# Kernel tuning notes

Measured on AMD Instinct MI355X. Metric: run time of the kernel, lower is better.

The kernel has to match this reference:

```python
import jax, jax.numpy as jnp
import numpy as np

T = 25
H1, H2, H3 = 16, 72, 32


def _lin_params(key, out_dim, in_dim):
    k1, k2 = jax.random.split(key)
    s = 1.0 / np.sqrt(in_dim)
    W = jax.random.uniform(k1, (out_dim, in_dim), jnp.float32, -s, s)
    b = jax.random.uniform(k2, (out_dim,), jnp.float32, -s, s)
    return W, b


def _lstm_params(key, in_dim, hid):
    k1, k2, k3, k4 = jax.random.split(key, 4)
    s = 1.0 / np.sqrt(hid)
    Wih = jax.random.uniform(k1, (4 * hid, in_dim), jnp.float32, -s, s)
    Whh = jax.random.uniform(k2, (4 * hid, hid), jnp.float32, -s, s)
    bih = jax.random.uniform(k3, (4 * hid,), jnp.float32, -s, s)
    bhh = jax.random.uniform(k4, (4 * hid,), jnp.float32, -s, s)
    return Wih, Whh, bih, bhh


def setup_inputs() -> dict:
    key = jax.random.key(0)
    ks = jax.random.split(key, 9)
    B = 131072
    x = jax.random.normal(ks[0], (B, T, 2), jnp.float32)
    y = jax.random.normal(ks[1], (B, T, 36), jnp.float32)
    Wih1, Whh1, bih1, bhh1 = _lstm_params(ks[2], 2, H1)
    Wih2, Whh2, bih2, bhh2 = _lstm_params(ks[3], H2, H2)
    Wih3, Whh3, bih3, bhh3 = _lstm_params(ks[4], H1 + H2, H3)
    W1, b1 = _lin_params(ks[5], 64, 36)
    W2, b2 = _lin_params(ks[6], H2, 64)
    W3, b3 = _lin_params(ks[7], 16, H3)
    W4, b4 = _lin_params(ks[8], 2, 16)
    return dict(x=x, y=y,
                Wih1=Wih1, Whh1=Whh1, bih1=bih1, bhh1=bhh1,
                Wih2=Wih2, Whh2=Whh2, bih2=bih2, bhh2=bhh2,
                Wih3=Wih3, Whh3=Whh3, bih3=bih3, bhh3=bhh3,
                W1=W1, b1=b1, W2=W2, b2=b2, W3=W3, b3=b3, W4=W4, b4=b4)


def _lstm_cell(xt, h, c, Wih, Whh, bih, bhh):
    # PyTorch LSTMCell gate order: i, f, g, o
    g = xt @ Wih.T + bih + h @ Whh.T + bhh
    i, f, gg, o = jnp.split(g, 4, axis=-1)
    c_new = jax.nn.sigmoid(f) * c + jax.nn.sigmoid(i) * jnp.tanh(gg)
    h_new = jax.nn.sigmoid(o) * jnp.tanh(c_new)
    return h_new, c_new


def _forward(x, y, Wih1, Whh1, bih1, bhh1, Wih2, Whh2, bih2, bhh2,
             Wih3, Whh3, bih3, bhh3, W1, b1, W2, b2, W3, b3, W4, b4):
    B = x.shape[0]
    init = (jnp.zeros((B, H1), jnp.float32), jnp.zeros((B, H1), jnp.float32),
            jnp.zeros((B, H2), jnp.float32), jnp.zeros((B, H2), jnp.float32),
            jnp.zeros((B, H3), jnp.float32), jnp.zeros((B, H3), jnp.float32))

    def step(carry, inp):
        h1, c1, h2, c2, h3, c3 = carry
        xt, yt = inp  # [B,2], [B,36]
        h1, c1 = _lstm_cell(xt, h1, c1, Wih1, Whh1, bih1, bhh1)
        l2 = jax.nn.relu(yt @ W1.T + b1) @ W2.T + b2
        h2, c2 = _lstm_cell(l2, h2, c2, Wih2, Whh2, bih2, bhh2)
        h = jnp.concatenate([h1, h2], axis=1)
        h3, c3 = _lstm_cell(h, h3, c3, Wih3, Whh3, bih3, bhh3)
        out = jax.nn.relu(h3 @ W3.T + b3) @ W4.T + b4  # [B,2]
        return (h1, c1, h2, c2, h3, c3), out

    xs = (jnp.swapaxes(x, 0, 1), jnp.swapaxes(y, 0, 1))  # [T,B,*]
    _, outs = jax.lax.scan(step, init, xs)  # [T,B,2]
    # torch.cat(outputs, dim=1) -> [B, T*2]
    return jnp.swapaxes(outs, 0, 1).reshape(B, T * 2)


def reference(x, y, Wih1, Whh1, bih1, bhh1, Wih2, Whh2, bih2, bhh2,
              Wih3, Whh3, bih3, bhh3, W1, b1, W2, b2, W3, b3, W4, b4):
    return _forward(x, y, Wih1, Whh1, bih1, bhh1, Wih2, Whh2, bih2, bhh2,
                    Wih3, Whh3, bih3, bhh3, W1, b1, W2, b2, W3, b3, W4, b4)
```

## Files before the change

### kernel.cpp

```cpp
#include <hip/hip_runtime.h>
#include <hip/hip_bf16.h>

#define THREADS 768

typedef __hip_bfloat16 bf16;
typedef __attribute__((ext_vector_type(4))) float f32x4;
typedef __attribute__((ext_vector_type(8))) short bf16x8;

#define MFMA __builtin_amdgcn_mfma_f32_16x16x32_bf16

#define O_A1  0
#define O_AY  4096
#define O_AT1 12288
#define O_A2  20480
#define O_AH3 40960
#define LDS_ELEMS 45056
#define LDS_BYTES (LDS_ELEMS * 2)

__device__ __forceinline__ int kmap(int l, int j) {
    return (((l >> 4) & 3) << 2) + (j & 3) + ((j >> 2) << 4);
}
__device__ __forceinline__ int frag_off(int m, int k) {
    int l = (m & 15) | (((k >> 2) & 3) << 4);
    int j = (k & 3) | (((k >> 4) & 1) << 2);
    return (l << 3) + j;
}
__device__ __forceinline__ void st_frag(bf16* sbase, int KC, int m, int k, float v) {
    sbase[(((m >> 4) * KC + (k >> 5)) << 9) + frag_off(m, k & 31)] = __float2bfloat16(v);
}
__device__ __forceinline__ void st_frag_c(bf16* sbase, int KC, int m, int cidx, int kl, float v) {
    sbase[(((m >> 4) * KC + cidx) << 9) + frag_off(m, kl)] = __float2bfloat16(v);
}

__device__ __forceinline__ float rcp_(float x) { return __builtin_amdgcn_rcpf(x); }

__device__ __forceinline__ float lstm_ew1(f32x4 acc, float& cst) {
    float ei = __expf(-acc[0]);
    float ef = __expf(-acc[1]);
    float eg = __expf(2.0f * fminf(acc[2], 40.0f));
    float eo = __expf(-acc[3]);
    float c = rcp_(1.0f + ef) * cst + (eg - 1.0f) * rcp_((1.0f + ei) * (eg + 1.0f));
    cst = c;
    float ec = __expf(2.0f * fminf(c, 40.0f));
    return (ec - 1.0f) * rcp_((1.0f + eo) * (ec + 1.0f));
}

__device__ __forceinline__ ushort bfu(float f) {
    union { bf16 b; ushort u; } v; v.b = __float2bfloat16(f); return v.u;
}

template <typename F>
__device__ __forceinline__ bf16x8 mk_frag(int lane, F val) {
    union { bf16x8 v; bf16 h[8]; } u;
#pragma unroll
    for (int j = 0; j < 8; ++j) u.h[j] = __float2bfloat16(val(kmap(lane, j)));
    return u.v;
}

__global__ void __launch_bounds__(THREADS, 3)
lstm_fused(const float* __restrict__ x, const float* __restrict__ y,
           const float* __restrict__ Wih1, const float* __restrict__ Whh1,
           const float* __restrict__ bih1, const float* __restrict__ bhh1,
           const float* __restrict__ Wih2, const float* __restrict__ Whh2,
           const float* __restrict__ bih2, const float* __restrict__ bhh2,
           const float* __restrict__ Wih3, const float* __restrict__ Whh3,
           const float* __restrict__ bih3, const float* __restrict__ bhh3,
           const float* __restrict__ W1, const float* __restrict__ b1,
           const float* __restrict__ W2, const float* __restrict__ b2,
           const float* __restrict__ W3, const float* __restrict__ b3,
           const float* __restrict__ W4, const float* __restrict__ b4,
           float* __restrict__ out) {
    extern __shared__ char smem[];
    bf16* sb = (bf16*)smem;
    const int tid = threadIdx.x;
    const int wave = tid >> 6, lane = tid & 63, ln15 = lane & 15;
    const int b0 = blockIdx.x * 64;

    const bool HEAVY = wave < 6;
    const int ntL2a = HEAVY ? 2 * wave : 6 + wave;

    bf16x8 bL2[2][5];
    bf16x8 bL1 = {};
    bf16x8 bF1[2] = {};
    bf16x8 bF2[2] = {};
    bf16x8 bL3[5] = {};
    bf16x8 bF3 = {};

    {
        auto fillL2 = [&](int nt, bf16x8* dst) {
            int R = (nt << 4) + ln15;
            int r = (R & 3) * 72 + (R >> 2);
            float bias = bih2[r] + bhh2[r];
#pragma unroll
            for (int kc = 0; kc < 5; ++kc)
                dst[kc] = mk_frag(lane, [&](int kl) {
                    int k = kc * 32 + kl;
                    return k < 72 ? Wih2[r * 72 + k]
                         : (k < 144 ? Whh2[r * 72 + (k - 72)]
                         : (k == 144 ? bias : 0.0f)); });
        };
        fillL2(ntL2a, bL2[0]);
        if (HEAVY) fillL2(2 * wave + 1, bL2[1]);
        else { bL2[1][0] = bL2[0][0]; bL2[1][1] = bL2[0][0]; bL2[1][2] = bL2[0][0];
               bL2[1][3] = bL2[0][0]; bL2[1][4] = bL2[0][0]; }
    }
    if (wave >= 6 && wave < 10) {
        int R = ((wave - 6) << 4) + ln15;
        int r = (R & 3) * 16 + (R >> 2);
        float bias = bih1[r] + bhh1[r];
        bL1 = mk_frag(lane, [&](int k) {
            return k < 2 ? Wih1[r * 2 + k]
                 : (k < 18 ? Whh1[r * 16 + (k - 2)]
                 : (k == 18 ? bias : 0.0f)); });
    }
    if (wave >= 8) {
        int n = ((wave - 8) << 4) + ln15;
        float bias = b1[n];
#pragma unroll
        for (int kc = 0; kc < 2; ++kc)
            bF1[kc] = mk_frag(lane, [&](int kl) {
                int k = kc * 32 + kl;
                return k < 36 ? W1[n * 36 + k] : (k == 36 ? bias : 0.0f); });
    }
    if (wave >= 4) {
        int R = ((wave - 4) << 4) + ln15;
        int r = (R & 3) * 32 + (R >> 2);
        float bias = bih3[r] + bhh3[r];
        bL3[0] = mk_frag(lane, [&](int k) {
            return (k >= 2 && k < 18) ? Wih3[r * 88 + (k - 2)] : (k == 18 ? bias : 0.0f); });
        bL3[1] = mk_frag(lane, [&](int k) {
            return (k >= 8) ? Wih3[r * 88 + 8 + k] : 0.0f; });
        bL3[2] = mk_frag(lane, [&](int k) { return Wih3[r * 88 + 40 + k]; });
        bL3[3] = mk_frag(lane, [&](int k) {
            return (k < 16) ? Wih3[r * 88 + 72 + k] : 0.0f; });
        bL3[4] = mk_frag(lane, [&](int k) { return Whh3[r * 32 + k]; });
    }
    if (wave < 4 || wave == 7) {
        int nt2 = (wave == 7) ? 4 : wave;
        int n = (nt2 << 4) + ln15;
#pragma unroll
        for (int kc = 0; kc < 2; ++kc)
            bF2[kc] = mk_frag(lane, [&](int kl) {
                return (n < 72) ? W2[n * 64 + kc * 32 + kl] : 0.0f; });
    }
    if (wave < 4) bF3 = mk_frag(lane, [&](int k) { return W3[ln15 * 32 + k]; });

    {
        int4* z = (int4*)sb;
        int4 zv = {0, 0, 0, 0};
        for (int i = tid; i < LDS_BYTES / 16; i += THREADS) z[i] = zv;
    }
    __syncthreads();
    for (int it = tid; it < 2 * 2304; it += THREADS) {
        int slot = it / 2304, r2 = it - slot * 2304;
        int m = r2 / 36, k = r2 - m * 36;
        st_frag(sb + O_AY + ((slot * 8) << 9), 2, m, k,
                y[(size_t)(b0 + m) * 900 + slot * 36 + k]);
    }
    if (tid < 128) {
        int m = tid >> 1, k = tid & 1;
        st_frag(sb + O_A1, 1, m, k, x[(size_t)(b0 + m) * 50 + k]);
    }
    {
        const bf16 one = __float2bfloat16(1.0f);
        if (tid < 128) {
            int s = tid >> 6, mt = (tid >> 4) & 3, n = tid & 15;
            sb[O_A1 + ((s * 4 + mt) << 9) + frag_off(n, 18)] = one;
        } else if (tid < 256) {
            int i = tid - 128; int s = i >> 6, mt = (i >> 4) & 3, n = i & 15;
            sb[O_AY + ((s * 8 + mt * 2 + 1) << 9) + frag_off(n, 4)] = one;
        } else if (tid < 384) {
            int i = tid - 256; int s = i >> 6, mt = (i >> 4) & 3, n = i & 15;
            sb[O_A2 + ((mt * 10 + 8 + s) << 9) + frag_off(n, 16)] = one;
        }
    }
    __syncthreads();
    if (wave >= 8) {
        const int nf0 = ((wave - 8) << 4) + ((lane >> 4) << 2);
#pragma unroll
        for (int s = 0; s < 2; ++s) {
#pragma unroll
            for (int mt = 0; mt < 4; ++mt) {
                f32x4 acc = {0.f, 0.f, 0.f, 0.f};
#pragma unroll
                for (int kc = 0; kc < 2; ++kc) {
                    bf16x8 a = *(const bf16x8*)(sb + O_AY + ((s * 8 + mt * 2 + kc) << 9) + (lane << 3));
                    acc = MFMA(bF1[kc], a, acc, 0, 0, 0);
                }
                int batch = (mt << 4) + ln15;
#pragma unroll
                for (int r = 0; r < 4; ++r)
                    st_frag(sb + O_AT1 + (((s ^ 1) * 8) << 9), 2, batch, nf0 + r, fmaxf(acc[r], 0.0f));
            }
        }
    }
    __syncthreads();
    if (wave < 4 || wave == 7) {
        const int nt2 = (wave == 7) ? 4 : wave;
        const int nb = (nt2 << 4) + ((lane >> 4) << 2);
        float4 bv = {0.f, 0.f, 0.f, 0.f};
        if (nb < 72) bv = *(const float4*)(b2 + nb);
#pragma unroll
        for (int mt = 0; mt < 4; ++mt) {
            f32x4 acc = {0.f, 0.f, 0.f, 0.f};
#pragma unroll
            for (int kc = 0; kc < 2; ++kc) {
                bf16x8 a = *(const bf16x8*)(sb + O_AT1 + ((8 + mt * 2 + kc) << 9) + (lane << 3));
                acc = MFMA(bF2[kc], a, acc, 0, 0, 0);
            }
            if (nb < 72) {
                int batch = (mt << 4) + ln15;
#pragma unroll
                for (int r = 0; r < 4; ++r) {
                    int n = nb + r;
                    st_frag_c(sb + O_A2, 10, batch, ((n >> 5) << 1), n & 31, acc[r] + bv[r]);
                }
            }
        }
    } else if (wave >= 10) {
        const int m = ((wave - 10) << 5) + (lane >> 1);
        const int mt = m >> 4;
        const float* yp = y + (size_t)(b0 + m) * 900 + 2 * 36;
#pragma unroll
        for (int c = (lane & 1); c < 9; c += 2) {
            float4 v = *(const float4*)(yp + 4 * c);
            ushort4 pk;
            pk.x = bfu(v.x); pk.y = bfu(v.y); pk.z = bfu(v.z); pk.w = bfu(v.w);
            int k0 = 4 * c, kc = k0 >> 5;
            int l2v = (m & 15) | (((k0 >> 2) & 3) << 4);
            int j0 = ((k0 >> 4) & 1) << 2;
            *(ushort4*)((ushort*)(sb + O_AY) + ((mt * 2 + kc) << 9) + (l2v << 3) + j0) = pk;
        }
    }
    float c1[4] = {};
    float cs2[2][4] = {};
    float c3[4] = {};
    __syncthreads();

    for (int t = 0; t <= 25; ++t) {
        const int p = t & 1, q = p ^ 1;

        if (t <= 24) {
#pragma unroll
            for (int mt = 0; mt < 4; ++mt) {
                bf16x8 al[5];
#pragma unroll
                for (int b = 0; b < 5; ++b)
                    al[b] = *(const bf16x8*)(sb + O_A2 + ((mt * 10 + 2 * b + p) << 9) + (lane << 3));
                {
                    f32x4 acc = {0.f, 0.f, 0.f, 0.f};
#pragma unroll
                    for (int b = 0; b < 5; ++b) acc = MFMA(bL2[0][b], al[b], acc, 0, 0, 0);
                    float hv = lstm_ew1(acc, cs2[0][mt]);
                    int batch = (mt << 4) + ln15;
                    int k = 72 + (ntL2a << 2) + (lane >> 4);
                    st_frag_c(sb + O_A2, 10, batch, ((k >> 5) << 1) + q, k & 31, hv);
                }
                if (HEAVY) {
                    f32x4 acc = {0.f, 0.f, 0.f, 0.f};
#pragma unroll
                    for (int b = 0; b < 5; ++b) acc = MFMA(bL2[1][b], al[b], acc, 0, 0, 0);
                    float hv = lstm_ew1(acc, cs2[1][mt]);
                    int batch = (mt << 4) + ln15;
                    int k = 72 + ((2 * wave + 1) << 2) + (lane >> 4);
                    st_frag_c(sb + O_A2, 10, batch, ((k >> 5) << 1) + q, k & 31, hv);
                }
            }
        }

        if (t <= 24 && wave >= 6 && wave < 10) {
            const int nt1 = wave - 6;
#pragma unroll
            for (int mt = 0; mt < 4; ++mt) {
                bf16x8 a = *(const bf16x8*)(sb + O_A1 + ((p * 4 + mt) << 9) + (lane << 3));
                f32x4 acc = {0.f, 0.f, 0.f, 0.f};
                acc = MFMA(bL1, a, acc, 0, 0, 0);
                float hv = lstm_ew1(acc, c1[mt]);
                int batch = (mt << 4) + ln15;
                st_frag(sb + O_A1 + ((q * 4) << 9), 1, batch, 2 + (nt1 << 2) + (lane >> 4), hv);
            }
        }
        if (wave == 6 && t <= 23) {
            const int m = lane, mt = m >> 4;
            float2 xv = *(const float2*)(x + (size_t)(b0 + m) * 50 + (t + 1) * 2);
            union { uint u; ushort s[2]; } xu;
            xu.s[0] = bfu(xv.x); xu.s[1] = bfu(xv.y);
            *(uint*)((ushort*)(sb + O_A1) + ((q * 4 + mt) << 9) + ((m & 15) << 3)) = xu.u;
        }
        if (t <= 22 && wave >= 8) {
            const int nf0 = ((wave - 8) << 4) + ((lane >> 4) << 2);
#pragma unroll
            for (int mt = 0; mt < 4; ++mt) {
                f32x4 acc = {0.f, 0.f, 0.f, 0.f};
#pragma unroll
                for (int kc = 0; kc < 2; ++kc) {
                    bf16x8 a = *(const bf16x8*)(sb + O_AY + ((p * 8 + mt * 2 + kc) << 9) + (lane << 3));
                    acc = MFMA(bF1[kc], a, acc, 0, 0, 0);
                }
                int batch = (mt << 4) + ln15;
#pragma unroll
                for (int r = 0; r < 4; ++r)
                    st_frag(sb + O_AT1 + ((q * 8) << 9), 2, batch, nf0 + r, fmaxf(acc[r], 0.0f));
            }
        }
        if (wave >= 10 && t <= 21) {
            const int m = ((wave - 10) << 5) + (lane >> 1);
            const int mt = m >> 4;
            const float* yp = y + (size_t)(b0 + m) * 900 + (t + 3) * 36;
#pragma unroll
            for (int c = (lane & 1); c < 9; c += 2) {
                float4 v = *(const float4*)(yp + 4 * c);
                ushort4 pk;
                pk.x = bfu(v.x); pk.y = bfu(v.y); pk.z = bfu(v.z); pk.w = bfu(v.w);
                int k0 = 4 * c, kc = k0 >> 5;
                int l2v = (m & 15) | (((k0 >> 2) & 3) << 4);
                int j0 = ((k0 >> 4) & 1) << 2;
                *(ushort4*)((ushort*)(sb + O_AY) + ((q * 8 + mt * 2 + kc) << 9) + (l2v << 3) + j0) = pk;
            }
        }
        if (t >= 1 && wave >= 4) {
            const int nt3 = wave - 4;
#pragma unroll
            for (int mt = 0; mt < 4; ++mt) {
                f32x4 acc = {0.f, 0.f, 0.f, 0.f};
                bf16x8 a0 = *(const bf16x8*)(sb + O_A1 + ((p * 4 + mt) << 9) + (lane << 3));
                acc = MFMA(bL3[0], a0, acc, 0, 0, 0);
#pragma unroll
                for (int j = 0; j < 3; ++j) {
                    bf16x8 a = *(const bf16x8*)(sb + O_A2 + ((mt * 10 + 4 + 2 * j + p) << 9) + (lane << 3));
                    acc = MFMA(bL3[1 + j], a, acc, 0, 0, 0);
                }
                bf16x8 a4 = *(const bf16x8*)(sb + O_AH3 + ((p * 4 + mt) << 9) + (lane << 3));
                acc = MFMA(bL3[4], a4, acc, 0, 0, 0);
                float hv = lstm_ew1(acc, c3[mt]);
                int batch = (mt << 4) + ln15;
                st_frag(sb + O_AH3 + ((q * 4) << 9), 1, batch, (nt3 << 2) + (lane >> 4), hv);
            }
        }
        if (t <= 23 && (wave < 4 || wave == 7)) {
            const int nt2 = (wave == 7) ? 4 : wave;
            const int nb = (nt2 << 4) + ((lane >> 4) << 2);
            float4 bv = {0.f, 0.f, 0.f, 0.f};
            if (nb < 72) bv = *(const float4*)(b2 + nb);
#pragma unroll
            for (int mt = 0; mt < 4; ++mt) {
                f32x4 acc = {0.f, 0.f, 0.f, 0.f};
#pragma unroll
                for (int kc = 0; kc < 2; ++kc) {
                    bf16x8 a = *(const bf16x8*)(sb + O_AT1 + ((p * 8 + mt * 2 + kc) << 9) + (lane << 3));
                    acc = MFMA(bF2[kc], a, acc, 0, 0, 0);
                }
                if (nb < 72) {
                    int batch = (mt << 4) + ln15;
#pragma unroll
                    for (int r = 0; r < 4; ++r) {
                        int n = nb + r;
                        st_frag_c(sb + O_A2, 10, batch, ((n >> 5) << 1) + q, n & 31, acc[r] + bv[r]);
                    }
                }
            }
        }
        if (t >= 2 && wave < 4) {
            const int mt = wave, qd = lane >> 4;
            float4 b3v = *(const float4*)(b3 + 4 * qd);
            float4 w0v = *(const float4*)(W4 + 4 * qd);
            float4 w1v = *(const float4*)(W4 + 16 + 4 * qd);
            bf16x8 bb = *(const bf16x8*)(sb + O_AH3 + ((p * 4 + mt) << 9) + (lane << 3));
            f32x4 acc = {0.f, 0.f, 0.f, 0.f};
            acc = MFMA(bF3, bb, acc, 0, 0, 0);
            float s0 = 0.f, s1 = 0.f;
#pragma unroll
            for (int r = 0; r < 4; ++r) {
                float u = fmaxf(acc[r] + b3v[r], 0.0f);
                s0 = fmaf(u, w0v[r], s0);
                s1 = fmaf(u, w1v[r], s1);
            }
            s0 += __shfl_xor(s0, 16); s0 += __shfl_xor(s0, 32);
            s1 += __shfl_xor(s1, 16); s1 += __shfl_xor(s1, 32);
            if (lane < 16) {
                float2 o; o.x = s0 + b4[0]; o.y = s1 + b4[1];
                *(float2*)(out + (size_t)(b0 + (mt << 4) + lane) * 50 + (t - 2) * 2) = o;
            }
        }
        __syncthreads();
    }

    if (wave < 4) {
        const int mt = wave, qd = lane >> 4;
        float4 b3v = *(const float4*)(b3 + 4 * qd);
        float4 w0v = *(const float4*)(W4 + 4 * qd);
        float4 w1v = *(const float4*)(W4 + 16 + 4 * qd);
        bf16x8 bb = *(const bf16x8*)(sb + O_AH3 + (mt << 9) + (lane << 3));
        f32x4 acc = {0.f, 0.f, 0.f, 0.f};
        acc = MFMA(bF3, bb, acc, 0, 0, 0);
        float s0 = 0.f, s1 = 0.f;
#pragma unroll
        for (int r = 0; r < 4; ++r) {
            float u = fmaxf(acc[r] + b3v[r], 0.0f);
            s0 = fmaf(u, w0v[r], s0);
            s1 = fmaf(u, w1v[r], s1);
        }
        s0 += __shfl_xor(s0, 16); s0 += __shfl_xor(s0, 32);
        s1 += __shfl_xor(s1, 16); s1 += __shfl_xor(s1, 32);
        if (lane < 16) {
            float2 o; o.x = s0 + b4[0]; o.y = s1 + b4[1];
            *(float2*)(out + (size_t)(b0 + (mt << 4) + lane) * 50 + 24 * 2) = o;
        }
    }
}

extern "C" void kernel_launch(void* const* d_in, const int* in_sizes, int n_in,
                              void* d_out, int out_size, void* d_ws, size_t ws_size,
                              hipStream_t stream) {
    (void)in_sizes; (void)n_in; (void)d_ws; (void)ws_size; (void)out_size;
    hipFuncSetAttribute((const void*)lstm_fused,
                        hipFuncAttributeMaxDynamicSharedMemorySize, LDS_BYTES);
    lstm_fused<<<dim3(2048), dim3(THREADS), LDS_BYTES, stream>>>(
        (const float*)d_in[0], (const float*)d_in[1],
        (const float*)d_in[2], (const float*)d_in[3],
        (const float*)d_in[4], (const float*)d_in[5],
        (const float*)d_in[6], (const float*)d_in[7],
        (const float*)d_in[8], (const float*)d_in[9],
        (const float*)d_in[10], (const float*)d_in[11],
        (const float*)d_in[12], (const float*)d_in[13],
        (const float*)d_in[14], (const float*)d_in[15],
        (const float*)d_in[16], (const float*)d_in[17],
        (const float*)d_in[18], (const float*)d_in[19],
        (const float*)d_in[20], (const float*)d_in[21],
        (float*)d_out);
}
```

Before: 1.001 ms.

## Rebalance LSTM work across 16 waves with unified per-wave weight register array

The block grows from 12 to 16 waves, and all layers' work is reassigned across them. L2 gate tiles now go to waves 0-13, L1 to waves 4-7 and L3 to waves 8-15, while the dense y→l2 path runs on waves 14-15 plus wave 4. Per-wave weight fragments are collapsed into a single 13-entry register array so that each wave holds only the fragments for its roles, keeping register pressure within the tighter 1024-thread launch bound. The goal is a shorter per-timestep critical path through better load balance, at the cost of more waves per block contending for the barriers and the MFMA units.

New measurement: 1.013 ms. No clear change (+1.1%).

```diff
diff --git a/kernel.cpp b/kernel.cpp
--- a/kernel.cpp
+++ b/kernel.cpp
@@ -1,7 +1,7 @@
 #include <hip/hip_runtime.h>
 #include <hip/hip_bf16.h>
 
-#define THREADS 768
+#define THREADS 1024
 
 typedef __hip_bfloat16 bf16;
 typedef __attribute__((ext_vector_type(4))) float f32x4;
@@ -57,7 +57,7 @@
     return u.v;
 }
 
-__global__ void __launch_bounds__(THREADS, 3)
+__global__ void __launch_bounds__(THREADS, 4)
 lstm_fused(const float* __restrict__ x, const float* __restrict__ y,
            const float* __restrict__ Wih1, const float* __restrict__ Whh1,
            const float* __restrict__ bih1, const float* __restrict__ bhh1,
@@ -76,74 +76,82 @@
     const int wave = tid >> 6, lane = tid & 63, ln15 = lane & 15;
     const int b0 = blockIdx.x * 64;
 
-    const bool HEAVY = wave < 6;
-    const int ntL2a = HEAVY ? 2 * wave : 6 + wave;
-
-    bf16x8 bL2[2][5];
-    bf16x8 bL1 = {};
-    bf16x8 bF1[2] = {};
-    bf16x8 bF2[2] = {};
-    bf16x8 bL3[5] = {};
-    bf16x8 bF3 = {};
+    bf16x8 W[13];
+#pragma unroll
+    for (int i = 0; i < 13; ++i) W[i] = bf16x8{0, 0, 0, 0, 0, 0, 0, 0};
 
     {
-        auto fillL2 = [&](int nt, bf16x8* dst) {
+        auto l2frag = [&](int nt, int kc) {
             int R = (nt << 4) + ln15;
             int r = (R & 3) * 72 + (R >> 2);
             float bias = bih2[r] + bhh2[r];
-#pragma unroll
-            for (int kc = 0; kc < 5; ++kc)
-                dst[kc] = mk_frag(lane, [&](int kl) {
-                    int k = kc * 32 + kl;
-                    return k < 72 ? Wih2[r * 72 + k]
-                         : (k < 144 ? Whh2[r * 72 + (k - 72)]
-                         : (k == 144 ? bias : 0.0f)); });
+            return mk_frag(lane, [&](int kl) {
+                int k = kc * 32 + kl;
+                return k < 72 ? Wih2[r * 72 + k]
+                     : (k < 144 ? Whh2[r * 72 + (k - 72)]
+                     : (k == 144 ? bias : 0.0f)); });
         };
-        fillL2(ntL2a, bL2[0]);
-        if (HEAVY) fillL2(2 * wave + 1, bL2[1]);
-        else { bL2[1][0] = bL2[0][0]; bL2[1][1] = bL2[0][0]; bL2[1][2] = bL2[0][0];
-               bL2[1][3] = bL2[0][0]; bL2[1][4] = bL2[0][0]; }
-    }
-    if (wave >= 6 && wave < 10) {
-        int R = ((wave - 6) << 4) + ln15;
+        if (wave < 4) {
+#pragma unroll
+            for (int kc = 0; kc < 5; ++kc) W[kc] = l2frag(2 * wave, kc);
+#pragma unroll
+            for (int kc = 0; kc < 5; ++kc) W[5 + kc] = l2frag(2 * wave + 1, kc);
+        } else if (wave < 14) {
+#pragma unroll
+            for (int kc = 0; kc < 5; ++kc) W[kc] = l2frag(wave + 4, kc);
+        }
+    }
+    if (wave >= 4 && wave < 8) {
+        int R = ((wave - 4) << 4) + ln15;
         int r = (R & 3) * 16 + (R >> 2);
         float bias = bih1[r] + bhh1[r];
-        bL1 = mk_frag(lane, [&](int k) {
+        W[5] = mk_frag(lane, [&](int k) {
             return k < 2 ? Wih1[r * 2 + k]
                  : (k < 18 ? Whh1[r * 16 + (k - 2)]
                  : (k == 18 ? bias : 0.0f)); });
     }
-    if (wave >= 8) {
-        int n = ((wave - 8) << 4) + ln15;
-        float bias = b1[n];
+    if (wave == 4) {
+        int n = 64 + ln15;
 #pragma unroll
         for (int kc = 0; kc < 2; ++kc)
-            bF1[kc] = mk_frag(lane, [&](int kl) {
-                int k = kc * 32 + kl;
-                return k < 36 ? W1[n * 36 + k] : (k == 36 ? bias : 0.0f); });
-    }
-    if (wave >= 4) {
-        int R = ((wave - 4) << 4) + ln15;
-        int r = (R & 3) * 32 + (R >> 2);
-        float bias = bih3[r] + bhh3[r];
-        bL3[0] = mk_frag(lane, [&](int k) {
-            return (k >= 2 && k < 18) ? Wih3[r * 88 + (k - 2)] : (k == 18 ? bias : 0.0f); });
-        bL3[1] = mk_frag(lane, [&](int k) {
-            return (k >= 8) ? Wih3[r * 88 + 8 + k] : 0.0f; });
-        bL3[2] = mk_frag(lane, [&](int k) { return Wih3[r * 88 + 40 + k]; });
-        bL3[3] = mk_frag(lane, [&](int k) {
-            return (k < 16) ? Wih3[r * 88 + 72 + k] : 0.0f; });
-        bL3[4] = mk_frag(lane, [&](int k) { return Whh3[r * 32 + k]; });
-    }
-    if (wave < 4 || wave == 7) {
-        int nt2 = (wave == 7) ? 4 : wave;
-        int n = (nt2 << 4) + ln15;
-#pragma unroll
-        for (int kc = 0; kc < 2; ++kc)
-            bF2[kc] = mk_frag(lane, [&](int kl) {
+            W[6 + kc] = mk_frag(lane, [&](int kl) {
                 return (n < 72) ? W2[n * 64 + kc * 32 + kl] : 0.0f; });
     }
-    if (wave < 4) bF3 = mk_frag(lane, [&](int k) { return W3[ln15 * 32 + k]; });
+    {
+        auto l3fill = [&](int base) {
+            int R = ((wave - 8) << 4) + ln15;
+            int r = (R & 3) * 32 + (R >> 2);
+            float bias = bih3[r] + bhh3[r];
+            W[base + 0] = mk_frag(lane, [&](int k) {
+                return (k >= 2 && k < 18) ? Wih3[r * 88 + (k - 2)] : (k == 18 ? bias : 0.0f); });
+            W[base + 1] = mk_frag(lane, [&](int k) {
+                return (k >= 8) ? Wih3[r * 88 + 8 + k] : 0.0f; });
+            W[base + 2] = mk_frag(lane, [&](int k) { return Wih3[r * 88 + 40 + k]; });
+            W[base + 3] = mk_frag(lane, [&](int k) {
+                return (k < 16) ? Wih3[r * 88 + 72 + k] : 0.0f; });
+            W[base + 4] = mk_frag(lane, [&](int k) { return Whh3[r * 32 + k]; });
+        };
+        if (wave >= 8 && wave < 14) l3fill(5);
+        else if (wave >= 14) l3fill(0);
+    }
+    if (wave >= 8 && wave < 12)
+        W[10] = mk_frag(lane, [&](int k) { return W3[ln15 * 32 + k]; });
+    if (wave >= 14) {
+#pragma unroll
+        for (int nn = 0; nn < 2; ++nn) {
+            int n = ((2 * (wave - 14) + nn) << 4) + ln15;
+            float bias = b1[n];
+#pragma unroll
+            for (int kc = 0; kc < 2; ++kc)
+                W[5 + 2 * nn + kc] = mk_frag(lane, [&](int kl) {
+                    int k = kc * 32 + kl;
+                    return k < 36 ? W1[n * 36 + k] : (k == 36 ? bias : 0.0f); });
+#pragma unroll
+            for (int kc = 0; kc < 2; ++kc)
+                W[9 + 2 * nn + kc] = mk_frag(lane, [&](int kl) {
+                    return W2[n * 64 + kc * 32 + kl]; });
+        }
+    }
 
     {
         int4* z = (int4*)sb;
@@ -175,40 +183,40 @@
         }
     }
     __syncthreads();
-    if (wave >= 8) {
-        const int nf0 = ((wave - 8) << 4) + ((lane >> 4) << 2);
-#pragma unroll
-        for (int s = 0; s < 2; ++s) {
+    if (wave >= 14) {
+#pragma unroll
+        for (int nn = 0; nn < 2; ++nn) {
+            const int nf0 = ((2 * (wave - 14) + nn) << 4) + ((lane >> 4) << 2);
+#pragma unroll
+            for (int s = 0; s < 2; ++s) {
+#pragma unroll
+                for (int mt = 0; mt < 4; ++mt) {
+                    f32x4 acc = {0.f, 0.f, 0.f, 0.f};
+                    bf16x8 a0 = *(const bf16x8*)(sb + O_AY + ((s * 8 + mt * 2 + 0) << 9) + (lane << 3));
+                    bf16x8 a1 = *(const bf16x8*)(sb + O_AY + ((s * 8 + mt * 2 + 1) << 9) + (lane << 3));
+                    acc = MFMA(W[5 + 2 * nn], a0, acc, 0, 0, 0);
+                    acc = MFMA(W[6 + 2 * nn], a1, acc, 0, 0, 0);
+                    int batch = (mt << 4) + ln15;
+#pragma unroll
+                    for (int r = 0; r < 4; ++r)
+                        st_frag(sb + O_AT1 + (((s ^ 1) * 8) << 9), 2, batch, nf0 + r, fmaxf(acc[r], 0.0f));
+                }
+            }
+        }
+    }
+    __syncthreads();
+    if (wave >= 14) {
+#pragma unroll
+        for (int nn = 0; nn < 2; ++nn) {
+            const int nb = ((2 * (wave - 14) + nn) << 4) + ((lane >> 4) << 2);
+            float4 bv = *(const float4*)(b2 + nb);
 #pragma unroll
             for (int mt = 0; mt < 4; ++mt) {
                 f32x4 acc = {0.f, 0.f, 0.f, 0.f};
-#pragma unroll
-                for (int kc = 0; kc < 2; ++kc) {
-                    bf16x8 a = *(const bf16x8*)(sb + O_AY + ((s * 8 + mt * 2 + kc) << 9) + (lane << 3));
-                    acc = MFMA(bF1[kc], a, acc, 0, 0, 0);
-                }
-                int batch = (mt << 4) + ln15;
-#pragma unroll
-                for (int r = 0; r < 4; ++r)
-                    st_frag(sb + O_AT1 + (((s ^ 1) * 8) << 9), 2, batch, nf0 + r, fmaxf(acc[r], 0.0f));
-            }
-        }
-    }
-    __syncthreads();
-    if (wave < 4 || wave == 7) {
-        const int nt2 = (wave == 7) ? 4 : wave;
-        const int nb = (nt2 << 4) + ((lane >> 4) << 2);
-        float4 bv = {0.f, 0.f, 0.f, 0.f};
-        if (nb < 72) bv = *(const float4*)(b2 + nb);
-#pragma unroll
-        for (int mt = 0; mt < 4; ++mt) {
-            f32x4 acc = {0.f, 0.f, 0.f, 0.f};
-#pragma unroll
-            for (int kc = 0; kc < 2; ++kc) {
-                bf16x8 a = *(const bf16x8*)(sb + O_AT1 + ((8 + mt * 2 + kc) << 9) + (lane << 3));
-                acc = MFMA(bF2[kc], a, acc, 0, 0, 0);
-            }
-            if (nb < 72) {
+                bf16x8 a0 = *(const bf16x8*)(sb + O_AT1 + ((8 + mt * 2 + 0) << 9) + (lane << 3));
+                bf16x8 a1 = *(const bf16x8*)(sb + O_AT1 + ((8 + mt * 2 + 1) << 9) + (lane << 3));
+                acc = MFMA(W[9 + 2 * nn], a0, acc, 0, 0, 0);
+                acc = MFMA(W[10 + 2 * nn], a1, acc, 0, 0, 0);
                 int batch = (mt << 4) + ln15;
 #pragma unroll
                 for (int r = 0; r < 4; ++r) {
@@ -217,8 +225,7 @@
                 }
             }
         }
-    } else if (wave >= 10) {
-        const int m = ((wave - 10) << 5) + (lane >> 1);
+        const int m = ((wave - 14) << 5) + (lane >> 1);
         const int mt = m >> 4;
         const float* yp = y + (size_t)(b0 + m) * 900 + 2 * 36;
 #pragma unroll
@@ -231,16 +238,58 @@
             int j0 = ((k0 >> 4) & 1) << 2;
             *(ushort4*)((ushort*)(sb + O_AY) + ((mt * 2 + kc) << 9) + (l2v << 3) + j0) = pk;
         }
-    }
-    float c1[4] = {};
-    float cs2[2][4] = {};
-    float c3[4] = {};
+    } else if (wave == 4) {
+        const int nb = 64 + ((lane >> 4) << 2);
+        float4 bv = {0.f, 0.f, 0.f, 0.f};
+        if (nb < 72) bv = *(const float4*)(b2 + nb);
+#pragma unroll
+        for (int mt = 0; mt < 4; ++mt) {
+            f32x4 acc = {0.f, 0.f, 0.f, 0.f};
+            bf16x8 a0 = *(const bf16x8*)(sb + O_AT1 + ((8 + mt * 2 + 0) << 9) + (lane << 3));
+            bf16x8 a1 = *(const bf16x8*)(sb + O_AT1 + ((8 + mt * 2 + 1) << 9) + (lane << 3));
+            acc = MFMA(W[6], a0, acc, 0, 0, 0);
+            acc = MFMA(W[7], a1, acc, 0, 0, 0);
+            if (nb < 72) {
+                int batch = (mt << 4) + ln15;
+#pragma unroll
+                for (int r = 0; r < 4; ++r) {
+                    int n = nb + r;
+                    st_frag_c(sb + O_A2, 10, batch, ((n >> 5) << 1), n & 31, acc[r] + bv[r]);
+                }
+            }
+        }
+    }
+    float cA[4] = {};
+    float cB[4] = {};
     __syncthreads();
+
+#define L3_BODY(W0, W1, W2_, W3_, W4_, CST)                                              \
+    {                                                                                     \
+        const int nt3 = wave - 8;                                                         \
+        _Pragma("unroll")                                                                 \
+        for (int mt = 0; mt < 4; ++mt) {                                                  \
+            f32x4 acc = {0.f, 0.f, 0.f, 0.f};                                             \
+            bf16x8 a0 = *(const bf16x8*)(sb + O_A1 + ((p * 4 + mt) << 9) + (lane << 3));  \
+            acc = MFMA(W0, a0, acc, 0, 0, 0);                                             \
+            bf16x8 a1 = *(const bf16x8*)(sb + O_A2 + ((mt * 10 + 4 + p) << 9) + (lane << 3)); \
+            acc = MFMA(W1, a1, acc, 0, 0, 0);                                             \
+            bf16x8 a2 = *(const bf16x8*)(sb + O_A2 + ((mt * 10 + 6 + p) << 9) + (lane << 3)); \
+            acc = MFMA(W2_, a2, acc, 0, 0, 0);                                            \
+            bf16x8 a3 = *(const bf16x8*)(sb + O_A2 + ((mt * 10 + 8 + p) << 9) + (lane << 3)); \
+            acc = MFMA(W3_, a3, acc, 0, 0, 0);                                            \
+            bf16x8 a4 = *(const bf16x8*)(sb + O_AH3 + ((p * 4 + mt) << 9) + (lane << 3)); \
+            acc = MFMA(W4_, a4, acc, 0, 0, 0);                                            \
+            float hv = lstm_ew1(acc, CST[mt]);                                            \
+            int batch = (mt << 4) + ln15;                                                 \
+            st_frag(sb + O_AH3 + ((q * 4) << 9), 1, batch, (nt3 << 2) + (lane >> 4), hv); \
+        }                                                                                 \
+    }
 
     for (int t = 0; t <= 25; ++t) {
         const int p = t & 1, q = p ^ 1;
 
-        if (t <= 24) {
+        if (t <= 24 && wave < 14) {
+            const int ntA = (wave < 4) ? 2 * wave : wave + 4;
 #pragma unroll
             for (int mt = 0; mt < 4; ++mt) {
                 bf16x8 al[5];
@@ -250,17 +299,17 @@
                 {
                     f32x4 acc = {0.f, 0.f, 0.f, 0.f};
 #pragma unroll
-                    for (int b = 0; b < 5; ++b) acc = MFMA(bL2[0][b], al[b], acc, 0, 0, 0);
-                    float hv = lstm_ew1(acc, cs2[0][mt]);
+                    for (int b = 0; b < 5; ++b) acc = MFMA(W[b], al[b], acc, 0, 0, 0);
+                    float hv = lstm_ew1(acc, cA[mt]);
                     int batch = (mt << 4) + ln15;
-                    int k = 72 + (ntL2a << 2) + (lane >> 4);
+                    int k = 72 + (ntA << 2) + (lane >> 4);
                     st_frag_c(sb + O_A2, 10, batch, ((k >> 5) << 1) + q, k & 31, hv);
                 }
-                if (HEAVY) {
+                if (wave < 4) {
                     f32x4 acc = {0.f, 0.f, 0.f, 0.f};
 #pragma unroll
-                    for (int b = 0; b < 5; ++b) acc = MFMA(bL2[1][b], al[b], acc, 0, 0, 0);
-                    float hv = lstm_ew1(acc, cs2[1][mt]);
+                    for (int b = 0; b < 5; ++b) acc = MFMA(W[5 + b], al[b], acc, 0, 0, 0);
+                    float hv = lstm_ew1(acc, cB[mt]);
                     int batch = (mt << 4) + ln15;
                     int k = 72 + ((2 * wave + 1) << 2) + (lane >> 4);
                     st_frag_c(sb + O_A2, 10, batch, ((k >> 5) << 1) + q, k & 31, hv);
@@ -268,43 +317,45 @@
             }
         }
 
-        if (t <= 24 && wave >= 6 && wave < 10) {
-            const int nt1 = wave - 6;
+        if (t <= 24 && wave >= 4 && wave < 8) {
+            const int nt1 = wave - 4;
 #pragma unroll
             for (int mt = 0; mt < 4; ++mt) {
                 bf16x8 a = *(const bf16x8*)(sb + O_A1 + ((p * 4 + mt) << 9) + (lane << 3));
                 f32x4 acc = {0.f, 0.f, 0.f, 0.f};
-                acc = MFMA(bL1, a, acc, 0, 0, 0);
-                float hv = lstm_ew1(acc, c1[mt]);
+                acc = MFMA(W[5], a, acc, 0, 0, 0);
+                float hv = lstm_ew1(acc, cB[mt]);
                 int batch = (mt << 4) + ln15;
                 st_frag(sb + O_A1 + ((q * 4) << 9), 1, batch, 2 + (nt1 << 2) + (lane >> 4), hv);
             }
         }
-        if (wave == 6 && t <= 23) {
+        if (wave == 5 && t <= 23) {
             const int m = lane, mt = m >> 4;
             float2 xv = *(const float2*)(x + (size_t)(b0 + m) * 50 + (t + 1) * 2);
             union { uint u; ushort s[2]; } xu;
             xu.s[0] = bfu(xv.x); xu.s[1] = bfu(xv.y);
             *(uint*)((ushort*)(sb + O_A1) + ((q * 4 + mt) << 9) + ((m & 15) << 3)) = xu.u;
         }
-        if (t <= 22 && wave >= 8) {
-            const int nf0 = ((wave - 8) << 4) + ((lane >> 4) << 2);
-#pragma unroll
-            for (int mt = 0; mt < 4; ++mt) {
-                f32x4 acc = {0.f, 0.f, 0.f, 0.f};
-#pragma unroll
-                for (int kc = 0; kc < 2; ++kc) {
-                    bf16x8 a = *(const bf16x8*)(sb + O_AY + ((p * 8 + mt * 2 + kc) << 9) + (lane << 3));
-                    acc = MFMA(bF1[kc], a, acc, 0, 0, 0);
-                }
-                int batch = (mt << 4) + ln15;
-#pragma unroll
-                for (int r = 0; r < 4; ++r)
-                    st_frag(sb + O_AT1 + ((q * 8) << 9), 2, batch, nf0 + r, fmaxf(acc[r], 0.0f));
-            }
-        }
-        if (wave >= 10 && t <= 21) {
-            const int m = ((wave - 10) << 5) + (lane >> 1);
+        if (t <= 22 && wave >= 14) {
+#pragma unroll
+            for (int nn = 0; nn < 2; ++nn) {
+                const int nf0 = ((2 * (wave - 14) + nn) << 4) + ((lane >> 4) << 2);
+#pragma unroll
+                for (int mt = 0; mt < 4; ++mt) {
+                    f32x4 acc = {0.f, 0.f, 0.f, 0.f};
+                    bf16x8 a0 = *(const bf16x8*)(sb + O_AY + ((p * 8 + mt * 2 + 0) << 9) + (lane << 3));
+                    bf16x8 a1 = *(const bf16x8*)(sb + O_AY + ((p * 8 + mt * 2 + 1) << 9) + (lane << 3));
+                    acc = MFMA(W[5 + 2 * nn], a0, acc, 0, 0, 0);
+                    acc = MFMA(W[6 + 2 * nn], a1, acc, 0, 0, 0);
+                    int batch = (mt << 4) + ln15;
+#pragma unroll
+                    for (int r = 0; r < 4; ++r)
+                        st_frag(sb + O_AT1 + ((q * 8) << 9), 2, batch, nf0 + r, fmaxf(acc[r], 0.0f));
+                }
+            }
+        }
+        if (wave >= 14 && t <= 21) {
+            const int m = ((wave - 14) << 5) + (lane >> 1);
             const int mt = m >> 4;
             const float* yp = y + (size_t)(b0 + m) * 900 + (t + 3) * 36;
 #pragma unroll
@@ -318,56 +369,61 @@
                 *(ushort4*)((ushort*)(sb + O_AY) + ((q * 8 + mt * 2 + kc) << 9) + (l2v << 3) + j0) = pk;
             }
         }
-        if (t >= 1 && wave >= 4) {
-            const int nt3 = wave - 4;
-#pragma unroll
-            for (int mt = 0; mt < 4; ++mt) {
-                f32x4 acc = {0.f, 0.f, 0.f, 0.f};
-                bf16x8 a0 = *(const bf16x8*)(sb + O_A1 + ((p * 4 + mt) << 9) + (lane << 3));
-                acc = MFMA(bL3[0], a0, acc, 0, 0, 0);
-#pragma unroll
-                for (int j = 0; j < 3; ++j) {
-                    bf16x8 a = *(const bf16x8*)(sb + O_A2 + ((mt * 10 + 4 + 2 * j + p) << 9) + (lane << 3));
-                    acc = MFMA(bL3[1 + j], a, acc, 0, 0, 0);
-                }
-                bf16x8 a4 = *(const bf16x8*)(sb + O_AH3 + ((p * 4 + mt) << 9) + (lane << 3));
-                acc = MFMA(bL3[4], a4, acc, 0, 0, 0);
-                float hv = lstm_ew1(acc, c3[mt]);
-                int batch = (mt << 4) + ln15;
-                st_frag(sb + O_AH3 + ((q * 4) << 9), 1, batch, (nt3 << 2) + (lane >> 4), hv);
-            }
-        }
-        if (t <= 23 && (wave < 4 || wave == 7)) {
-            const int nt2 = (wave == 7) ? 4 : wave;
-            const int nb = (nt2 << 4) + ((lane >> 4) << 2);
-            float4 bv = {0.f, 0.f, 0.f, 0.f};
-            if (nb < 72) bv = *(const float4*)(b2 + nb);
-#pragma unroll
-            for (int mt = 0; mt < 4; ++mt) {
-                f32x4 acc = {0.f, 0.f, 0.f, 0.f};
-#pragma unroll
-                for (int kc = 0; kc < 2; ++kc) {
-                    bf16x8 a = *(const bf16x8*)(sb + O_AT1 + ((p * 8 + mt * 2 + kc) << 9) + (lane << 3));
-                    acc = MFMA(bF2[kc], a, acc, 0, 0, 0);
-                }
-                if (nb < 72) {
-                    int batch = (mt << 4) + ln15;
-#pragma unroll
-                    for (int r = 0; r < 4; ++r) {
-                        int n = nb + r;
-                        st_frag_c(sb + O_A2, 10, batch, ((n >> 5) << 1) + q, n & 31, acc[r] + bv[r]);
+        if (t >= 1 && wave >= 8) {
+            if (wave < 14) L3_BODY(W[5], W[6], W[7], W[8], W[9], cB)
+            else           L3_BODY(W[0], W[1], W[2], W[3], W[4], cA)
+        }
+        if (t <= 23) {
+            if (wave >= 14) {
+#pragma unroll
+                for (int nn = 0; nn < 2; ++nn) {
+                    const int nb = ((2 * (wave - 14) + nn) << 4) + ((lane >> 4) << 2);
+                    float4 bv = *(const float4*)(b2 + nb);
+#pragma unroll
+                    for (int mt = 0; mt < 4; ++mt) {
+                        f32x4 acc = {0.f, 0.f, 0.f, 0.f};
+                        bf16x8 a0 = *(const bf16x8*)(sb + O_AT1 + ((p * 8 + mt * 2 + 0) << 9) + (lane << 3));
+                        bf16x8 a1 = *(const bf16x8*)(sb + O_AT1 + ((p * 8 + mt * 2 + 1) << 9) + (lane << 3));
+                        acc = MFMA(W[9 + 2 * nn], a0, acc, 0, 0, 0);
+                        acc = MFMA(W[10 + 2 * nn], a1, acc, 0, 0, 0);
+                        int batch = (mt << 4) + ln15;
+#pragma unroll
+                        for (int r = 0; r < 4; ++r) {
+                            int n = nb + r;
+                            st_frag_c(sb + O_A2, 10, batch, ((n >> 5) << 1) + q, n & 31, acc[r] + bv[r]);
+                        }
                     }
                 }
-            }
-        }
-        if (t >= 2 && wave < 4) {
-            const int mt = wave, qd = lane >> 4;
+            } else if (wave == 4) {
+                const int nb = 64 + ((lane >> 4) << 2);
+                float4 bv = {0.f, 0.f, 0.f, 0.f};
+                if (nb < 72) bv = *(const float4*)(b2 + nb);
+#pragma unroll
+                for (int mt = 0; mt < 4; ++mt) {
+                    f32x4 acc = {0.f, 0.f, 0.f, 0.f};
+                    bf16x8 a0 = *(const bf16x8*)(sb + O_AT1 + ((p * 8 + mt * 2 + 0) << 9) + (lane << 3));
+                    bf16x8 a1 = *(const bf16x8*)(sb + O_AT1 + ((p * 8 + mt * 2 + 1) << 9) + (lane << 3));
+                    acc = MFMA(W[6], a0, acc, 0, 0, 0);
+                    acc = MFMA(W[7], a1, acc, 0, 0, 0);
+                    if (nb < 72) {
+                        int batch = (mt << 4) + ln15;
+#pragma unroll
+                        for (int r = 0; r < 4; ++r) {
+                            int n = nb + r;
+                            st_frag_c(sb + O_A2, 10, batch, ((n >> 5) << 1) + q, n & 31, acc[r] + bv[r]);
+                        }
+                    }
+                }
+            }
+        }
+        if (t >= 2 && wave >= 8 && wave < 12) {
+            const int mt = wave - 8, qd = lane >> 4;
             float4 b3v = *(const float4*)(b3 + 4 * qd);
             float4 w0v = *(const float4*)(W4 + 4 * qd);
             float4 w1v = *(const float4*)(W4 + 16 + 4 * qd);
             bf16x8 bb = *(const bf16x8*)(sb + O_AH3 + ((p * 4 + mt) << 9) + (lane << 3));
             f32x4 acc = {0.f, 0.f, 0.f, 0.f};
-            acc = MFMA(bF3, bb, acc, 0, 0, 0);
+            acc = MFMA(W[10], bb, acc, 0, 0, 0);
             float s0 = 0.f, s1 = 0.f;
 #pragma unroll
             for (int r = 0; r < 4; ++r) {
@@ -385,14 +441,14 @@
         __syncthreads();
     }
 
-    if (wave < 4) {
-        const int mt = wave, qd = lane >> 4;
+    if (wave >= 8 && wave < 12) {
+        const int mt = wave - 8, qd = lane >> 4;
         float4 b3v = *(const float4*)(b3 + 4 * qd);
         float4 w0v = *(const float4*)(W4 + 4 * qd);
         float4 w1v = *(const float4*)(W4 + 16 + 4 * qd);
         bf16x8 bb = *(const bf16x8*)(sb + O_AH3 + (mt << 9) + (lane << 3));
         f32x4 acc = {0.f, 0.f, 0.f, 0.f};
-        acc = MFMA(bF3, bb, acc, 0, 0, 0);
+        acc = MFMA(W[10], bb, acc, 0, 0, 0);
         float s0 = 0.f, s1 = 0.f;
 #pragma unroll
         for (int r = 0; r < 4; ++r) {
```
